# Kernel tuning notes

Hardware: AMD Instinct MI355X
Metric: run time of the kernel (lower is better)

Reference implementation:

```python
import jax, jax.numpy as jnp
import numpy as np

BN_EPS = 1e-5


def _gcn(x, A, W, gamma, beta):
    # x: [B,N,Cin], A: [B,N,N] -> [B,N,Cout]; BatchNorm1d over (B,N) per channel (train-mode batch stats)
    h = jnp.einsum('bnm,bmc->bnc', A, x @ W)
    mu = h.mean(axis=(0, 1))
    var = h.var(axis=(0, 1))
    h = (h - mu) * jax.lax.rsqrt(var + BN_EPS) * gamma + beta
    return jax.nn.relu(h)  # dropout is identity (drop_prob=0 / eval)


def _ppige(x, A, W0, g0, b0, W_res, g_res, b_res):
    h = _gcn(x, A, W0, g0, b0)
    for i in range(W_res.shape[0]):  # residual GCN stack (num_GCN-1 layers)
        h = _gcn(h, A, W_res[i], g_res[i], b_res[i]) + h
    return h


def _gge(x, w1, b1, w2, b2):
    return jax.nn.relu(jax.nn.relu(x @ w1 + b1) @ w2 + b2)


def _gaga(G, h):
    # G: [B,N,H], h: [B,H]
    att = jax.nn.softmax(jnp.einsum('bnh,bh->bn', G, h), axis=-1)
    return jnp.einsum('bnh,bn->bh', G, att)


def _led(ea, eb, conv_w, conv_b, p1_w, p1_b, p2_w, p2_b):
    # ea, eb: [B, 2H]; Conv1d(2H->2H, k=1) over length-2 axis then MaxPool1d(2)
    stacked = jnp.stack([ea, eb], axis=-1)  # [B, 2H, 2]
    conv = jnp.einsum('oc,bct->bot', conv_w, stacked) + conv_b[None, :, None]
    cnn_x = conv.max(axis=-1)  # [B, 2H]
    x = jax.nn.relu(jnp.concatenate([cnn_x, ea - eb], axis=1) @ p1_w + p1_b)
    return x @ p2_w + p2_b


def setup_inputs() -> dict:
    key = jax.random.key(0)
    ks = jax.random.split(key, 24)
    Bs, N, PPI_in, H, F_in = 8, 2048, 512, 256, 1024
    n_res = 3  # num_GCN - 1
    s = 0.02
    adjA = jax.random.uniform(ks[0], (Bs, N, N), jnp.float32)
    adjB = jax.random.uniform(ks[1], (Bs, N, N), jnp.float32)
    adjA = adjA / adjA.sum(-1, keepdims=True)  # row-normalized for numerical sanity
    adjB = adjB / adjB.sum(-1, keepdims=True)
    return {
        'a': jax.random.normal(ks[2], (Bs, F_in), jnp.float32),
        'bio_a': jax.random.normal(ks[3], (Bs, N, PPI_in), jnp.float32),
        'A': adjA,
        'b': jax.random.normal(ks[4], (Bs, F_in), jnp.float32),
        'bio_b': jax.random.normal(ks[5], (Bs, N, PPI_in), jnp.float32),
        'B': adjB,
        'W0': jax.random.normal(ks[6], (PPI_in, H), jnp.float32) * s,
        'gamma0': jnp.ones((H,), jnp.float32),
        'beta0': jnp.zeros((H,), jnp.float32),
        'W_res': jax.random.normal(ks[7], (n_res, H, H), jnp.float32) * s,
        'gamma_res': jnp.ones((n_res, H), jnp.float32),
        'beta_res': jnp.zeros((n_res, H), jnp.float32),
        'g1_w': jax.random.normal(ks[8], (F_in, 128), jnp.float32) * s,
        'g1_b': jnp.zeros((128,), jnp.float32),
        'g2_w': jax.random.normal(ks[9], (128, H), jnp.float32) * s,
        'g2_b': jnp.zeros((H,), jnp.float32),
        'conv_w': jax.random.normal(ks[10], (2 * H, 2 * H), jnp.float32) * s,
        'conv_b': jnp.zeros((2 * H,), jnp.float32),
        'p1_w': jax.random.normal(ks[11], (4 * H, H), jnp.float32) * s,
        'p1_b': jnp.zeros((H,), jnp.float32),
        'p2_w': jax.random.normal(ks[12], (H, 2), jnp.float32) * s,
        'p2_b': jnp.zeros((2,), jnp.float32),
    }


def reference(a, bio_a, A, b, bio_b, B, W0, gamma0, beta0, W_res, gamma_res, beta_res,
              g1_w, g1_b, g2_w, g2_b, conv_w, conv_b, p1_w, p1_b, p2_w, p2_b):
    Ga = _ppige(bio_a, A, W0, gamma0, beta0, W_res, gamma_res, beta_res)
    Gb = _ppige(bio_b, B, W0, gamma0, beta0, W_res, gamma_res, beta_res)
    ha = _gge(a, g1_w, g1_b, g2_w, g2_b)
    hb = _gge(b, g1_w, g1_b, g2_w, g2_b)
    ea = jnp.concatenate([ha, _gaga(Ga, ha)], axis=-1)
    eb = jnp.concatenate([hb, _gaga(Gb, hb)], axis=-1)
    logits = _led(ea, eb, conv_w, conv_b, p1_w, p1_b, p2_w, p2_b)
    return jax.nn.log_softmax(logits, axis=-1)
```

## Files before the change

### kernel.cpp

```cpp
#include <hip/hip_runtime.h>
#include <hip/hip_bf16.h>
#include <cstdint>

typedef unsigned short u16;
typedef __bf16 bf16x8 __attribute__((ext_vector_type(8)));
typedef float f32x4 __attribute__((ext_vector_type(4)));

typedef __attribute__((address_space(1))) const void* gas_ptr;
typedef __attribute__((address_space(3))) void* las_ptr;

__device__ __forceinline__ u16 f2bf(float f) {
  union { __hip_bfloat16 h; u16 u; } v;
  v.h = __float2bfloat16(f);
  return v.u;
}
__device__ __forceinline__ float bf2f(u16 u) {
  union { unsigned int i; float f; } v;
  v.i = ((unsigned int)u) << 16;
  return v.f;
}

__device__ __forceinline__ void gload16(const u16* g, u16* l) {
  __builtin_amdgcn_global_load_lds((gas_ptr)g, (las_ptr)l, 16, 0, 0);
}

__global__ __launch_bounds__(256) void k_prep_weights(const float* __restrict__ W0,
                                                      const float* __restrict__ Wres,
                                                      u16* __restrict__ W0t,
                                                      u16* __restrict__ Wrt) {
  __shared__ float tile[32][33];
  int y = blockIdx.y;
  const float* src; u16* dst; int R, r0;
  if (y < 16) { src = W0; dst = W0t; R = 512; r0 = y * 32; }
  else {
    int i = (y - 16) >> 3;
    src = Wres + i * 65536; dst = Wrt + i * 65536; R = 256; r0 = ((y - 16) & 7) * 32;
  }
  const int C = 256;
  int c0 = blockIdx.x * 32;
  int tx = threadIdx.x & 31, ty = threadIdx.x >> 5;
#pragma unroll
  for (int i = 0; i < 4; ++i) {
    int r = ty + i * 8;
    tile[r][tx] = src[(long)(r0 + r) * C + c0 + tx];
  }
  __syncthreads();
#pragma unroll
  for (int i = 0; i < 4; ++i) {
    int c = ty + i * 8;
    dst[(long)(c0 + c) * R + r0 + tx] = f2bf(tile[tx][c]);
  }
}

template<int EPI, int CVT>
__global__ __launch_bounds__(512) void k_gemm(
    const u16* __restrict__ A, int lda, long sA,
    const float* __restrict__ Afa, const float* __restrict__ Afb,
    long splitRow, int ldaf, long zrows, u16* __restrict__ AbfOut,
    const u16* __restrict__ Bt, int ldb, long sB,
    u16* __restrict__ C, int ldc, long sC,
    u16* __restrict__ PtOut, int ldpt,
    float* __restrict__ stats, int K) {
  __shared__ __align__(16) u16 smem[49152];
  __shared__ float cs[512];
  const int tid = threadIdx.x;
  const int lane = tid & 63;
  const int wid = tid >> 6;
  const int wm = wid >> 2, wn = wid & 3;

  int bx = blockIdx.x, bz = blockIdx.z;
  {
    int nx = gridDim.x;
    int tiles = nx * gridDim.z;
    int lin = bx + nx * bz;
    int chunk = tiles >> 3;
    int swz = (lin & 7) * chunk + (lin >> 3);
    bx = swz % nx; bz = swz / nx;
  }
  const long m0 = (long)bx * 128;
  const int z = bz;
  const u16* Ab = A + (long)z * sA;
  const u16* Btb = Bt + (long)z * sB;

  const int rsub = lane >> 3;
  const int swzcol = ((lane & 7) ^ rsub) * 8;
  const long a_row = m0 + wid * 16 + rsub;
  const int b_row = wid * 32 + rsub;

  if (EPI == 0) cs[tid] = 0.f;

  const f32x4 zero = {0.f, 0.f, 0.f, 0.f};
  f32x4 acc[4][4];
#pragma unroll
  for (int i = 0; i < 4; ++i)
#pragma unroll
    for (int j = 0; j < 4; ++j) acc[i][j] = zero;

  const int fr = lane & 15;
  const int kgrp = lane >> 4;
  const int swz_rd = lane & 7;
  const int nk = K >> 6;

  float4 rgf[4];

  auto stageA = [&](int bufofs, int k0) {
#pragma unroll
    for (int i = 0; i < 2; ++i)
      gload16(Ab + (a_row + i * 8) * (long)lda + (k0 + swzcol),
              &smem[bufofs + (wid * 16 + i * 8) * 64]);
  };
  auto stageB = [&](int bufofs, int k0) {
#pragma unroll
    for (int i = 0; i < 4; ++i)
      gload16(Btb + (long)(b_row + i * 8) * ldb + (k0 + swzcol),
              &smem[bufofs + (wid * 32 + i * 8) * 64]);
  };
  auto loadA = [&](int k0) {
#pragma unroll
    for (int i = 0; i < 2; ++i) {
      long R = (long)z * zrows + a_row + i * 8;
      const float* sp = (R < splitRow ? Afa + R * (long)ldaf
                                      : Afb + (R - splitRow) * (long)ldaf) + k0 + swzcol;
      rgf[i * 2] = *reinterpret_cast<const float4*>(sp);
      rgf[i * 2 + 1] = *reinterpret_cast<const float4*>(sp + 4);
    }
  };
  auto writeA = [&](int bufofs, int k0) {
#pragma unroll
    for (int i = 0; i < 2; ++i) {
      union { u16 u[8]; uint4 qq; } o;
      o.u[0] = f2bf(rgf[i*2].x);   o.u[1] = f2bf(rgf[i*2].y);
      o.u[2] = f2bf(rgf[i*2].z);   o.u[3] = f2bf(rgf[i*2].w);
      o.u[4] = f2bf(rgf[i*2+1].x); o.u[5] = f2bf(rgf[i*2+1].y);
      o.u[6] = f2bf(rgf[i*2+1].z); o.u[7] = f2bf(rgf[i*2+1].w);
      if (AbfOut) {
        long R = (long)z * zrows + a_row + i * 8;
        *reinterpret_cast<uint4*>(AbfOut + R * (long)ldaf + k0 + swzcol) = o.qq;
      }
      *reinterpret_cast<uint4*>(&smem[bufofs + (wid * 16 + i * 8) * 64 + lane * 8]) = o.qq;
    }
  };
  auto compute = [&](const u16* Asb, const u16* Bsb) {
#pragma unroll
    for (int ks = 0; ks < 2; ++ks) {
      bf16x8 af[4], bfv[4];
#pragma unroll
      for (int f = 0; f < 4; ++f) {
        int cA = (ks * 4 + kgrp) ^ swz_rd;
        af[f]  = *reinterpret_cast<const bf16x8*>(&Asb[(wm * 64 + f * 16 + fr) * 64 + cA * 8]);
        bfv[f] = *reinterpret_cast<const bf16x8*>(&Bsb[(wn * 64 + f * 16 + fr) * 64 + cA * 8]);
      }
#pragma unroll
      for (int mf = 0; mf < 4; ++mf)
#pragma unroll
        for (int nf = 0; nf < 4; ++nf)
          acc[mf][nf] = __builtin_amdgcn_mfma_f32_16x16x32_bf16(af[mf], bfv[nf], acc[mf][nf], 0, 0, 0);
    }
  };

  if constexpr (CVT) {
    loadA(0); stageB(16384, 0); writeA(0, 0);
    for (int t = 0; t < nk; ++t) {
      int cur = t & 1, nxt = cur ^ 1;
      if (t + 1 < nk) {
        loadA((t + 1) * 64);
        stageB(16384 + nxt * 16384, (t + 1) * 64);
        asm volatile("s_waitcnt vmcnt(8) lgkmcnt(0)" ::: "memory");
      } else {
        asm volatile("s_waitcnt vmcnt(0) lgkmcnt(0)" ::: "memory");
      }
      __builtin_amdgcn_s_barrier();
      __builtin_amdgcn_sched_barrier(0);
      compute(&smem[cur * 8192], &smem[16384 + cur * 16384]);
      if (t + 1 < nk) writeA(nxt * 8192, (t + 1) * 64);
      asm volatile("s_waitcnt lgkmcnt(0)" ::: "memory");
      __builtin_amdgcn_s_barrier();
    }
  } else {
    stageA(0, 0); stageB(16384, 0);
    for (int t = 0; t < nk; ++t) {
      int cur = t & 1, nxt = cur ^ 1;
      if (t + 1 < nk) {
        stageA(nxt * 8192, (t + 1) * 64);
        stageB(16384 + nxt * 16384, (t + 1) * 64);
        asm volatile("s_waitcnt vmcnt(6) lgkmcnt(0)" ::: "memory");
      } else {
        asm volatile("s_waitcnt vmcnt(0) lgkmcnt(0)" ::: "memory");
      }
      __builtin_amdgcn_s_barrier();
      __builtin_amdgcn_sched_barrier(0);
      compute(&smem[cur * 8192], &smem[16384 + cur * 16384]);
      asm volatile("s_waitcnt lgkmcnt(0)" ::: "memory");
      __builtin_amdgcn_s_barrier();
    }
  }

  if (EPI == 0) {
    u16* Cb = C + (long)z * sC;
    const int side = z >> 3;
#pragma unroll
    for (int mf = 0; mf < 4; ++mf) {
      long mrow = m0 + wm * 64 + mf * 16 + kgrp * 4;
#pragma unroll
      for (int nf = 0; nf < 4; ++nf) {
        int ncol = wn * 64 + nf * 16 + fr;
#pragma unroll
        for (int r = 0; r < 4; ++r)
          Cb[(mrow + r) * ldc + ncol] = f2bf(acc[mf][nf][r]);
      }
    }
#pragma unroll
    for (int nf = 0; nf < 4; ++nf) {
      int cl = wn * 64 + nf * 16 + fr;
      float s = 0.f, q = 0.f;
#pragma unroll
      for (int mf = 0; mf < 4; ++mf)
#pragma unroll
        for (int r = 0; r < 4; ++r) { float v = acc[mf][nf][r]; s += v; q += v * v; }
      atomicAdd(&cs[cl], s);
      atomicAdd(&cs[256 + cl], q);
    }
    __syncthreads();
    atomicAdd(&stats[side * 512 + tid], cs[tid]);
  } else {
    u16* Ts = &smem[0];
#pragma unroll
    for (int mf = 0; mf < 4; ++mf)
#pragma unroll
      for (int nf = 0; nf < 4; ++nf) {
        int nl = wn * 64 + nf * 16 + fr;
        int ml = wm * 64 + mf * 16 + kgrp * 4;
#pragma unroll
        for (int r = 0; r < 4; ++r)
          Ts[nl * 136 + ml + r] = f2bf(acc[mf][nf][r]);
      }
    __syncthreads();
    int n = tid >> 1, half = tid & 1;
    const u16* sp = Ts + n * 136 + half * 64;
    u16* dp = PtOut + (long)n * ldpt + m0 + half * 64;
#pragma unroll
    for (int j = 0; j < 8; ++j)
      reinterpret_cast<uint4*>(dp)[j] = reinterpret_cast<const uint4*>(sp)[j];
  }
}

__global__ __launch_bounds__(256) void k_bn_apply(const ushort4* __restrict__ u4,
                                                  ushort4* __restrict__ h4,
                                                  const float* __restrict__ statsL,
                                                  const float* __restrict__ gamma,
                                                  const float* __restrict__ beta, int res) {
  long i = (long)blockIdx.x * 256 + threadIdx.x;
  int side = (int)(i >> 20);
  int c0 = (int)(i & 63) * 4;
  const float* st = statsL + side * 512;
  ushort4 uv = u4[i];
  float vp[4] = { bf2f(uv.x), bf2f(uv.y), bf2f(uv.z), bf2f(uv.w) };
  float rp[4];
#pragma unroll
  for (int j = 0; j < 4; ++j) {
    int c = c0 + j;
    float mu = st[c] * (1.f / 16384.f);
    float var = st[256 + c] * (1.f / 16384.f) - mu * mu;
    float sc = gamma[c] * rsqrtf(var + 1e-5f);
    float sh = beta[c] - mu * sc;
    rp[j] = fmaxf(vp[j] * sc + sh, 0.f);
  }
  if (res) {
    ushort4 hv = h4[i];
    rp[0] += bf2f(hv.x); rp[1] += bf2f(hv.y); rp[2] += bf2f(hv.z); rp[3] += bf2f(hv.w);
  }
  ushort4 o;
  o.x = f2bf(rp[0]); o.y = f2bf(rp[1]); o.z = f2bf(rp[2]); o.w = f2bf(rp[3]);
  h4[i] = o;
}

__global__ __launch_bounds__(256) void k_gge(const float* __restrict__ in_a,
                                             const float* __restrict__ in_b,
                                             const float* __restrict__ w1, const float* __restrict__ b1,
                                             const float* __restrict__ w2, const float* __restrict__ b2,
                                             float* __restrict__ ha) {
  __shared__ float av[1024];
  __shared__ float hid[128];
  int bx = blockIdx.x, t = threadIdx.x;
  const float* ap = ((bx >> 3) ? in_b : in_a) + (bx & 7) * 1024;
  for (int i = t; i < 1024; i += 256) av[i] = ap[i];
  __syncthreads();
  if (t < 128) {
    float s = b1[t];
    for (int c = 0; c < 1024; ++c) s += av[c] * w1[c * 128 + t];
    hid[t] = fmaxf(s, 0.f);
  }
  __syncthreads();
  float s = b2[t];
  for (int c = 0; c < 128; ++c) s += hid[c] * w2[c * 256 + t];
  ha[bx * 256 + t] = fmaxf(s, 0.f);
}

__global__ __launch_bounds__(256) void k_gaga_scores(const u16* __restrict__ h,
                                                     const float* __restrict__ ha,
                                                     float* __restrict__ sc) {
  __shared__ __align__(16) float has[256];
  int bx = blockIdx.x;
  has[threadIdx.x] = ha[bx * 256 + threadIdx.x];
  __syncthreads();
  const u16* G = h + (long)bx * 524288;
  int wv = threadIdx.x >> 6, lane = threadIdx.x & 63;
  float4 h4 = reinterpret_cast<const float4*>(has)[lane];
  for (int i = 0; i < 32; ++i) {
    int n = blockIdx.y * 128 + wv * 32 + i;
    ushort4 v = reinterpret_cast<const ushort4*>(G + (long)n * 256)[lane];
    float d = bf2f(v.x) * h4.x + bf2f(v.y) * h4.y + bf2f(v.z) * h4.z + bf2f(v.w) * h4.w;
#pragma unroll
    for (int o2 = 32; o2 > 0; o2 >>= 1) d += __shfl_down(d, o2);
    if (lane == 0) sc[bx * 2048 + n] = d;
  }
}

__global__ __launch_bounds__(256) void k_softmax2048(const float* __restrict__ sc, float* __restrict__ att) {
  __shared__ float red[256];
  int b = blockIdx.x, t = threadIdx.x;
  const float* s = sc + b * 2048;
  float* o = att + b * 2048;
  float v[8];
  float m = -1e30f;
#pragma unroll
  for (int i = 0; i < 8; ++i) { v[i] = s[t + i * 256]; m = fmaxf(m, v[i]); }
  red[t] = m; __syncthreads();
  for (int o2 = 128; o2 > 0; o2 >>= 1) { if (t < o2) red[t] = fmaxf(red[t], red[t + o2]); __syncthreads(); }
  m = red[0]; __syncthreads();
  float sum = 0.f;
#pragma unroll
  for (int i = 0; i < 8; ++i) { v[i] = expf(v[i] - m); sum += v[i]; }
  red[t] = sum; __syncthreads();
  for (int o2 = 128; o2 > 0; o2 >>= 1) { if (t < o2) red[t] += red[t + o2]; __syncthreads(); }
  float inv = 1.f / red[0];
#pragma unroll
  for (int i = 0; i < 8; ++i) o[t + i * 256] = v[i] * inv;
}

__global__ __launch_bounds__(256) void k_gaga_out(const u16* __restrict__ h,
                                                  const float* __restrict__ att,
                                                  float* __restrict__ ga) {
  __shared__ float atts[128];
  int bx = blockIdx.x, n0 = blockIdx.y * 128, c = threadIdx.x;
  if (threadIdx.x < 128) atts[threadIdx.x] = att[bx * 2048 + n0 + threadIdx.x];
  __syncthreads();
  const u16* base = h + (long)bx * 524288 + (long)n0 * 256 + c;
  float s = 0.f;
#pragma unroll 4
  for (int i = 0; i < 128; ++i) s += bf2f(base[(long)i * 256]) * atts[i];
  atomicAdd(&ga[bx * 256 + c], s);
}

__global__ __launch_bounds__(512) void k_led_conv(const float* __restrict__ ha, const float* __restrict__ ga,
                                                  const float* __restrict__ hb, const float* __restrict__ gb,
                                                  const float* __restrict__ cw, const float* __restrict__ cb,
                                                  float* __restrict__ cnn, float* __restrict__ diff) {
  __shared__ float ea[8][512], eb[8][512];
  int t = threadIdx.x;
  for (int i = t; i < 4096; i += 512) {
    int b = i >> 9, c = i & 511;
    float va = (c < 256) ? ha[b * 256 + c] : ga[b * 256 + c - 256];
    float vb = (c < 256) ? hb[b * 256 + c] : gb[b * 256 + c - 256];
    ea[b][c] = va; eb[b][c] = vb;
    if (blockIdx.x == 0) diff[i] = va - vb;
  }
  __syncthreads();
  int o = blockIdx.x * 64 + (t >> 3), b = t & 7;
  const float* wr = cw + (long)o * 512;
  float s0 = cb[o], s1 = s0;
  for (int c = 0; c < 512; ++c) { float w = wr[c]; s0 += w * ea[b][c]; s1 += w * eb[b][c]; }
  cnn[b * 512 + o] = fmaxf(s0, s1);
}

__global__ __launch_bounds__(256) void k_led_p1(const float* __restrict__ cnn, const float* __restrict__ diff,
                                                const float* __restrict__ w, const float* __restrict__ pb,
                                                float* __restrict__ x) {
  __shared__ float cat[8][1024];
  int t = threadIdx.x;
  for (int i = t; i < 8192; i += 256) {
    int b = i >> 10, c = i & 1023;
    cat[b][c] = (c < 512) ? cnn[b * 512 + c] : diff[b * 512 + c - 512];
  }
  __syncthreads();
  int o = blockIdx.x * 32 + (t >> 3), b = t & 7;
  float s = pb[o];
  for (int c = 0; c < 1024; ++c) s += cat[b][c] * w[c * 256 + o];
  x[b * 256 + o] = fmaxf(s, 0.f);
}

__global__ __launch_bounds__(64) void k_led_final(const float* __restrict__ x,
                                                  const float* __restrict__ p2w, const float* __restrict__ p2b,
                                                  float* __restrict__ out) {
  __shared__ float lg[16];
  int t = threadIdx.x;
  if (t < 16) {
    int b = t >> 1, j = t & 1;
    float s = p2b[j];
    for (int c = 0; c < 256; ++c) s += x[b * 256 + c] * p2w[c * 2 + j];
    lg[t] = s;
  }
  __syncthreads();
  if (t < 8) {
    float l0 = lg[t * 2], l1 = lg[t * 2 + 1];
    float m = fmaxf(l0, l1);
    float lse = m + logf(expf(l0 - m) + expf(l1 - m));
    out[t * 2] = l0 - lse;
    out[t * 2 + 1] = l1 - lse;
  }
}

extern "C" void kernel_launch(void* const* d_in, const int* in_sizes, int n_in,
                              void* d_out, int out_size, void* d_ws, size_t ws_size,
                              hipStream_t stream) {
  const float* in_a   = (const float*)d_in[0];
  const float* bio_a  = (const float*)d_in[1];
  const float* adj_a  = (const float*)d_in[2];
  const float* in_b   = (const float*)d_in[3];
  const float* bio_b  = (const float*)d_in[4];
  const float* adj_b  = (const float*)d_in[5];
  const float* W0     = (const float*)d_in[6];
  const float* gamma0 = (const float*)d_in[7];
  const float* beta0  = (const float*)d_in[8];
  const float* W_res  = (const float*)d_in[9];
  const float* g_res  = (const float*)d_in[10];
  const float* b_res  = (const float*)d_in[11];
  const float* g1_w   = (const float*)d_in[12];
  const float* g1_b   = (const float*)d_in[13];
  const float* g2_w   = (const float*)d_in[14];
  const float* g2_b   = (const float*)d_in[15];
  const float* conv_w = (const float*)d_in[16];
  const float* conv_b = (const float*)d_in[17];
  const float* p1_w   = (const float*)d_in[18];
  const float* p1_b   = (const float*)d_in[19];
  const float* p2_w   = (const float*)d_in[20];
  const float* p2_b   = (const float*)d_in[21];
  float* out = (float*)d_out;

  char* ws = (char*)d_ws;
  size_t off = 0;
  auto alloc = [&](size_t bytes) {
    char* p = ws + off;
    off += (bytes + 255) & ~(size_t)255;
    return p;
  };
  u16*   Abf   = (u16*)  alloc(67108864ull * 2);
  u16*   Pt    = (u16*)  alloc(8388608ull * 2);
  u16*   ubf   = (u16*)  alloc(8388608ull * 2);
  u16*   hbf   = (u16*)  alloc(8388608ull * 2);
  u16*   W0t   = (u16*)  alloc(131072ull * 2);
  u16*   Wrt   = (u16*)  alloc(196608ull * 2);
  float* stats = (float*)alloc(4096 * 4);
  float* gabuf = (float*)alloc(4096 * 4);
  float* hav   = (float*)alloc(4096 * 4);
  float* scb   = (float*)alloc(32768 * 4);
  float* attb  = (float*)alloc(32768 * 4);
  float* cnn   = (float*)alloc(4096 * 4);
  float* diff  = (float*)alloc(4096 * 4);
  float* xbuf  = (float*)alloc(2048 * 4);

  k_prep_weights<<<dim3(8, 40), 256, 0, stream>>>(W0, W_res, W0t, Wrt);
  (void)hipMemsetAsync(stats, 0, 32768, stream);

  for (int layer = 0; layer < 4; ++layer) {
    float* statsL = stats + layer * 1024;
    const float* gm = (layer == 0) ? gamma0 : (g_res + (layer - 1) * 256);
    const float* bt = (layer == 0) ? beta0 : (b_res + (layer - 1) * 256);

    if (layer == 0) {
      k_gemm<1, 1><<<dim3(256, 1, 1), 512, 0, stream>>>(
          nullptr, 0, 0, bio_a, bio_b, 16384L, 512, 0, nullptr,
          W0t, 512, 0, nullptr, 0, 0, Pt, 32768, nullptr, 512);
      k_gemm<0, 1><<<dim3(16, 1, 16), 512, 0, stream>>>(
          nullptr, 0, 0, adj_a, adj_b, 16384L, 2048, 2048, Abf,
          Pt, 32768, 2048, ubf, 256, 524288L, nullptr, 0, statsL, 2048);
    } else {
      const u16* Wt = Wrt + (layer - 1) * 65536;
      k_gemm<1, 0><<<dim3(256, 1, 1), 512, 0, stream>>>(
          hbf, 256, 0, nullptr, nullptr, 0, 0, 0, nullptr,
          Wt, 256, 0, nullptr, 0, 0, Pt, 32768, nullptr, 256);
      k_gemm<0, 0><<<dim3(16, 1, 16), 512, 0, stream>>>(
          Abf, 2048, 4194304L, nullptr, nullptr, 0, 0, 0, nullptr,
          Pt, 32768, 2048, ubf, 256, 524288L, nullptr, 0, statsL, 2048);
    }
    k_bn_apply<<<8192, 256, 0, stream>>>((const ushort4*)ubf, (ushort4*)hbf,
                                         statsL, gm, bt, layer ? 1 : 0);
  }

  k_gge<<<16, 256, 0, stream>>>(in_a, in_b, g1_w, g1_b, g2_w, g2_b, hav);
  k_gaga_scores<<<dim3(16, 16), 256, 0, stream>>>(hbf, hav, scb);
  k_softmax2048<<<16, 256, 0, stream>>>(scb, attb);
  k_gaga_out<<<dim3(16, 16), 256, 0, stream>>>(hbf, attb, gabuf);

  k_led_conv<<<8, 512, 0, stream>>>(hav, gabuf, hav + 2048, gabuf + 2048, conv_w, conv_b, cnn, diff);
  k_led_p1<<<8, 256, 0, stream>>>(cnn, diff, p1_w, p1_b, xbuf);
  k_led_final<<<1, 64, 0, stream>>>(xbuf, p2_w, p2_b, out);
}
```

Baseline: 561.0 us.

## Deepen GEMM pipeline to three stages with one barrier per K-step

Enlarges shared memory to hold three B (and A for the non-convert path) stages and prefetches two K-tiles ahead instead of one. This removes the second barrier per iteration, because the slot being overwritten is never the one being read. The convert path double-buffers fp32 register tiles (even/odd) so global loads stay in flight across two iterations. It uses more LDS (about 144KB per block) and more registers, which may cut occupancy, and relies on nk being even for the unrolled loop.

```diff
diff --git a/kernel.cpp b/kernel.cpp
--- a/kernel.cpp
+++ b/kernel.cpp
@@ -61,7 +61,7 @@
     u16* __restrict__ C, int ldc, long sC,
     u16* __restrict__ PtOut, int ldpt,
     float* __restrict__ stats, int K) {
-  __shared__ __align__(16) u16 smem[49152];
+  __shared__ __align__(16) u16 smem[73728];
   __shared__ float cs[512];
   const int tid = threadIdx.x;
   const int lane = tid & 63;
@@ -101,46 +101,46 @@
   const int swz_rd = lane & 7;
   const int nk = K >> 6;
 
-  float4 rgf[4];
-
-  auto stageA = [&](int bufofs, int k0) {
+  auto stageA = [&](int slot, int k0) {
 #pragma unroll
     for (int i = 0; i < 2; ++i)
       gload16(Ab + (a_row + i * 8) * (long)lda + (k0 + swzcol),
-              &smem[bufofs + (wid * 16 + i * 8) * 64]);
+              &smem[slot * 8192 + (wid * 16 + i * 8) * 64]);
   };
-  auto stageB = [&](int bufofs, int k0) {
+  auto stageB = [&](int slot, int k0) {
 #pragma unroll
     for (int i = 0; i < 4; ++i)
       gload16(Btb + (long)(b_row + i * 8) * ldb + (k0 + swzcol),
-              &smem[bufofs + (wid * 32 + i * 8) * 64]);
+              &smem[24576 + slot * 16384 + (wid * 32 + i * 8) * 64]);
   };
-  auto loadA = [&](int k0) {
+  auto loadA = [&](float4* rg, int k0) {
 #pragma unroll
     for (int i = 0; i < 2; ++i) {
       long R = (long)z * zrows + a_row + i * 8;
       const float* sp = (R < splitRow ? Afa + R * (long)ldaf
                                       : Afb + (R - splitRow) * (long)ldaf) + k0 + swzcol;
-      rgf[i * 2] = *reinterpret_cast<const float4*>(sp);
-      rgf[i * 2 + 1] = *reinterpret_cast<const float4*>(sp + 4);
+      rg[i * 2] = *reinterpret_cast<const float4*>(sp);
+      rg[i * 2 + 1] = *reinterpret_cast<const float4*>(sp + 4);
     }
   };
-  auto writeA = [&](int bufofs, int k0) {
+  auto writeA = [&](int slot, const float4* rg, int k0) {
 #pragma unroll
     for (int i = 0; i < 2; ++i) {
       union { u16 u[8]; uint4 qq; } o;
-      o.u[0] = f2bf(rgf[i*2].x);   o.u[1] = f2bf(rgf[i*2].y);
-      o.u[2] = f2bf(rgf[i*2].z);   o.u[3] = f2bf(rgf[i*2].w);
-      o.u[4] = f2bf(rgf[i*2+1].x); o.u[5] = f2bf(rgf[i*2+1].y);
-      o.u[6] = f2bf(rgf[i*2+1].z); o.u[7] = f2bf(rgf[i*2+1].w);
+      o.u[0] = f2bf(rg[i*2].x);   o.u[1] = f2bf(rg[i*2].y);
+      o.u[2] = f2bf(rg[i*2].z);   o.u[3] = f2bf(rg[i*2].w);
+      o.u[4] = f2bf(rg[i*2+1].x); o.u[5] = f2bf(rg[i*2+1].y);
+      o.u[6] = f2bf(rg[i*2+1].z); o.u[7] = f2bf(rg[i*2+1].w);
       if (AbfOut) {
         long R = (long)z * zrows + a_row + i * 8;
         *reinterpret_cast<uint4*>(AbfOut + R * (long)ldaf + k0 + swzcol) = o.qq;
       }
-      *reinterpret_cast<uint4*>(&smem[bufofs + (wid * 16 + i * 8) * 64 + lane * 8]) = o.qq;
+      *reinterpret_cast<uint4*>(&smem[slot * 8192 + (wid * 16 + i * 8) * 64 + lane * 8]) = o.qq;
     }
   };
-  auto compute = [&](const u16* Asb, const u16* Bsb) {
+  auto compute = [&](int aslot, int bslot) {
+    const u16* Asb = &smem[aslot * 8192];
+    const u16* Bsb = &smem[24576 + bslot * 16384];
 #pragma unroll
     for (int ks = 0; ks < 2; ++ks) {
       bf16x8 af[4], bfv[4];
@@ -159,43 +159,50 @@
   };
 
   if constexpr (CVT) {
-    loadA(0); stageB(16384, 0); writeA(0, 0);
-    for (int t = 0; t < nk; ++t) {
-      int cur = t & 1, nxt = cur ^ 1;
+    float4 rgE[4], rgO[4];
+    loadA(rgE, 0);
+    loadA(rgO, 64);
+    stageB(0, 0);
+    stageB(1, 64);
+    writeA(0, rgE, 0);
+    auto body = [&](int t, float4* loadDst, const float4* writeSrc) {
+      if (t + 2 < nk) loadA(loadDst, (t + 2) * 64);
       if (t + 1 < nk) {
-        loadA((t + 1) * 64);
-        stageB(16384 + nxt * 16384, (t + 1) * 64);
-        asm volatile("s_waitcnt vmcnt(8) lgkmcnt(0)" ::: "memory");
+        asm volatile("s_waitcnt vmcnt(10) lgkmcnt(0)" ::: "memory");
       } else {
         asm volatile("s_waitcnt vmcnt(0) lgkmcnt(0)" ::: "memory");
       }
       __builtin_amdgcn_s_barrier();
       __builtin_amdgcn_sched_barrier(0);
-      compute(&smem[cur * 8192], &smem[16384 + cur * 16384]);
-      if (t + 1 < nk) writeA(nxt * 8192, (t + 1) * 64);
-      asm volatile("s_waitcnt lgkmcnt(0)" ::: "memory");
-      __builtin_amdgcn_s_barrier();
+      if (t + 2 < nk) stageB((t + 2) % 3, (t + 2) * 64);
+      compute(t & 1, t % 3);
+      if (t + 1 < nk) writeA((t + 1) & 1, writeSrc, (t + 1) * 64);
+    };
+    for (int t = 0; t < nk; t += 2) {
+      body(t, rgE, rgO);
+      body(t + 1, rgO, rgE);
     }
   } else {
-    stageA(0, 0); stageB(16384, 0);
+    stageA(0, 0); stageB(0, 0);
+    stageA(1, 64); stageB(1, 64);
     for (int t = 0; t < nk; ++t) {
-      int cur = t & 1, nxt = cur ^ 1;
       if (t + 1 < nk) {
-        stageA(nxt * 8192, (t + 1) * 64);
-        stageB(16384 + nxt * 16384, (t + 1) * 64);
-        asm volatile("s_waitcnt vmcnt(6) lgkmcnt(0)" ::: "memory");
+        asm volatile("s_waitcnt vmcnt(6)" ::: "memory");
       } else {
-        asm volatile("s_waitcnt vmcnt(0) lgkmcnt(0)" ::: "memory");
+        asm volatile("s_waitcnt vmcnt(0)" ::: "memory");
       }
       __builtin_amdgcn_s_barrier();
       __builtin_amdgcn_sched_barrier(0);
-      compute(&smem[cur * 8192], &smem[16384 + cur * 16384]);
-      asm volatile("s_waitcnt lgkmcnt(0)" ::: "memory");
-      __builtin_amdgcn_s_barrier();
+      if (t + 2 < nk) {
+        stageA((t + 2) % 3, (t + 2) * 64);
+        stageB((t + 2) % 3, (t + 2) * 64);
+      }
+      compute(t % 3, t % 3);
     }
   }
 
   if (EPI == 0) {
+    __syncthreads();
     u16* Cb = C + (long)z * sC;
     const int side = z >> 3;
 #pragma unroll
@@ -223,6 +230,7 @@
     __syncthreads();
     atomicAdd(&stats[side * 512 + tid], cs[tid]);
   } else {
+    __syncthreads();
     u16* Ts = &smem[0];
 #pragma unroll
     for (int mf = 0; mf < 4; ++mf)
```

Result: slower. 577.4 us (+2.9%).
